# Performance work log

Hardware: AMD Instinct MI355X
Metric: run time of the kernel (lower is better)

## Reference

```python
import jax, jax.numpy as jnp
import numpy as np

K_SIZE = 7   # min_kernel_size (Parameter init value, clamped)
DIL = 2      # min_dilation (Parameter init value, clamped)


def conv2d(x, w, b):
    # x: (B, Cin, H, W), w: (Cout, Cin, kh, kw), stride 1, pad 1
    y = jax.lax.conv_general_dilated(
        x, w, window_strides=(1, 1), padding=((1, 1), (1, 1)),
        dimension_numbers=("NCHW", "OIHW", "NCHW"))
    return y + b[None, :, None, None]


def sincos_1d(length, dim, dtype):
    # standard sinusoidal encoding: (length, dim)
    half = dim // 2
    inv_freq = 1.0 / (10000.0 ** (jnp.arange(half, dtype=dtype) * 2.0 / dim))
    ang = jnp.arange(length, dtype=dtype)[:, None] * inv_freq[None, :]
    return jnp.concatenate([jnp.sin(ang), jnp.cos(ang)], axis=-1)


def positional_encoding_2d(H, W, C, dtype):
    # first C//2 channels encode height, last C//2 encode width -> (H, W, C)
    pe_h = sincos_1d(H, C // 2, dtype)  # (H, C/2)
    pe_w = sincos_1d(W, C // 2, dtype)  # (W, C/2)
    pe = jnp.concatenate([
        jnp.broadcast_to(pe_h[:, None, :], (H, W, C // 2)),
        jnp.broadcast_to(pe_w[None, :, :], (H, W, C // 2)),
    ], axis=-1)
    return pe


def na_indices(L, K, D):
    # NATTEN-style dilated neighborhood indices with border clamping.
    # Each position i attends within its dilation group g = i % D.
    i = jnp.arange(L)
    g = i % D
    r = i // D                       # rank within group
    Lg = (L - g + D - 1) // D        # group length
    start = jnp.clip(r - K // 2, 0, Lg - K)
    return g[:, None] + (start[:, None] + jnp.arange(K)[None, :]) * D  # (L, K)


def neighborhood_attention_2d(q, k, v, K, D):
    # q, k: (B, H, W, Cqk); v: (B, H, W, Cv); single head, scale = Cqk**-0.5
    B, H, W, Cqk = q.shape
    scale = jnp.asarray(Cqk, q.dtype) ** -0.5
    idx_h = na_indices(H, K, D)  # (H, K)
    idx_w = na_indices(W, K, D)  # (W, K)
    # gather neighborhood keys/values: (B, H, K, W, K, C)
    kn = k[:, idx_h][:, :, :, idx_w]
    vn = v[:, idx_h][:, :, :, idx_w]
    logits = jnp.einsum('bhwc,bhiwjc->bhwij', q * scale, kn)  # (B,H,W,K,K)
    p = jax.nn.softmax(logits.reshape(B, H, W, K * K), axis=-1)
    p = p.reshape(B, H, W, K, K)
    return jnp.einsum('bhwij,bhiwjc->bhwc', p, vn)


def setup_inputs() -> dict:
    key = jax.random.key(0)
    ks = jax.random.split(key, 4)
    B, Cin, H, W = 2, 64, 96, 96
    Ci, Co = 64, 128
    fan = Cin * 9
    s = (1.0 / fan) ** 0.5
    return {
        "x": jax.random.normal(ks[0], (B, Cin, H, W), dtype=jnp.float32),
        "wq": jax.random.normal(ks[1], (Ci, Cin, 3, 3), dtype=jnp.float32) * s,
        "bq": jnp.zeros((Ci,), dtype=jnp.float32),
        "wk": jax.random.normal(ks[2], (Ci, Cin, 3, 3), dtype=jnp.float32) * s,
        "bk": jnp.zeros((Ci,), dtype=jnp.float32),
        "wv": jax.random.normal(ks[3], (Co, Cin, 3, 3), dtype=jnp.float32) * s,
        "bv": jnp.zeros((Co,), dtype=jnp.float32),
    }


def reference(x, wq, bq, wk, bk, wv, bv):
    # Conv QKV (NCHW), then move to channels-last for attention
    q = jnp.transpose(conv2d(x, wq, bq), (0, 2, 3, 1))  # (B,H,W,Ci)
    k = jnp.transpose(conv2d(x, wk, bk), (0, 2, 3, 1))
    v = jnp.transpose(conv2d(x, wv, bv), (0, 2, 3, 1))  # (B,H,W,Co)
    B, H, W, Ci = q.shape
    pe = positional_encoding_2d(H, W, Ci, q.dtype)       # (H,W,Ci)
    pe_b = jnp.broadcast_to(pe[None], (B, H, W, Ci))
    q = jnp.concatenate([q, pe_b], axis=-1)              # (B,H,W,2*Ci)
    k = jnp.concatenate([k, pe_b], axis=-1)
    return neighborhood_attention_2d(q, k, v, K_SIZE, DIL)
```

## Files before the change

kernel.cpp:

```cpp
#include <hip/hip_runtime.h>
#include <math.h>

#define HWDIM 96
#define NPIX (HWDIM*HWDIM)
#define BATCH 2
#define CIN 64
#define CCAT 128
#define PADW 98

typedef __attribute__((ext_vector_type(8))) short bf16x8;
typedef __attribute__((ext_vector_type(4))) float f32x4;

__device__ __forceinline__ unsigned short f2bf(float f) {
    unsigned u = __builtin_bit_cast(unsigned, f);
    unsigned r = (u + 0x7FFFu + ((u >> 16) & 1u)) >> 16;
    return (unsigned short)r;
}

__global__ __launch_bounds__(256) void prep_kernel(
        const float* __restrict__ x,
        const float* __restrict__ wq, const float* __restrict__ wk,
        const float* __restrict__ wv,
        unsigned short* __restrict__ xp, unsigned short* __restrict__ wbT) {
    int bid = blockIdx.x;
    int tid = threadIdx.x;
    if (bid < BATCH * PADW) {
        __shared__ float xls[64][97];
        int b  = bid / PADW;
        int hp = bid % PADW;
        bool interior = (hp >= 1 && hp <= HWDIM);
        if (interior) {
            int h = hp - 1;
            for (int idx = tid; idx < 64 * HWDIM; idx += 256) {
                int ci = idx / HWDIM;
                int w  = idx % HWDIM;
                xls[ci][w] = x[((b * CIN + ci) * HWDIM + h) * HWDIM + w];
            }
        }
        __syncthreads();
        for (int idx = tid; idx < PADW * 64; idx += 256) {
            int wp = idx / 64;
            int ci = idx % 64;
            float v = 0.f;
            if (interior && wp >= 1 && wp <= HWDIM) v = xls[ci][wp - 1];
            xp[((b * PADW + hp) * PADW + wp) * 64 + ci] = f2bf(v);
        }
    } else {
        int base = (bid - BATCH * PADW) * 4096;
        #pragma unroll
        for (int e = 0; e < 16; ++e) {
            int idx = base + e * 256 + tid;
            int t   = idx / (256 * 64);
            int rem = idx % (256 * 64);
            int co  = rem / 64;
            int ci  = rem % 64;
            float val;
            if (co < 64)        val = wq[(co * 64 + ci) * 9 + t];
            else if (co < 128)  val = wk[((co - 64) * 64 + ci) * 9 + t];
            else                val = wv[((co - 128) * 64 + ci) * 9 + t];
            wbT[(t * 256 + co) * 64 + ci] = f2bf(val);
        }
    }
}

__global__ __launch_bounds__(256, 2) void conv_mfma(
        const unsigned short* __restrict__ xp,
        const unsigned short* __restrict__ wbT,
        const float* __restrict__ bq, const float* __restrict__ bk,
        const float* __restrict__ bv,
        unsigned short* __restrict__ Qb, unsigned short* __restrict__ Kb,
        unsigned short* __restrict__ Vb) {
    __shared__ unsigned short xs[3 * 50 * 72];
    int bx      = blockIdx.x;
    int spatial = (bx & 7) * 48 + (bx >> 3);
    int b    = spatial / 192;
    int hh   = spatial % 192;
    int h    = hh >> 1;
    int w0   = (hh & 1) * 48;
    int co0  = blockIdx.y * 128;
    int tid  = threadIdx.x;

    {
        uint4 rv[5];
        int   ldst[5];
        #pragma unroll
        for (int i = 0; i < 5; ++i) {
            int idx = tid + i * 256;
            bool valid = (i < 4) || (tid < 176);
            int r    = idx / 400;
            int rem  = idx % 400;
            int wp50 = rem >> 3;
            int c8   = rem & 7;
            if (valid)
                rv[i] = *(const uint4*)&xp[(((b * PADW) + h + r) * PADW + w0 + wp50) * 64 + c8 * 8];
            ldst[i] = (r * 50 + wp50) * 72 + c8 * 8;
        }
        #pragma unroll
        for (int i = 0; i < 5; ++i) {
            bool valid = (i < 4) || (tid < 176);
            if (valid) *(uint4*)&xs[ldst[i]] = rv[i];
        }
    }
    __syncthreads();

    int lane = tid & 63;
    int wv   = tid >> 6;
    int lw   = lane & 15;
    int ksub = (lane >> 4) * 8;
    int co_t = co0 + wv * 32;

    f32x4 acc[3][2];
    #pragma unroll
    for (int m = 0; m < 3; ++m)
        #pragma unroll
        for (int n = 0; n < 2; ++n) acc[m][n] = (f32x4){0.f, 0.f, 0.f, 0.f};

    #pragma unroll
    for (int half = 0; half < 2; ++half) {
        bf16x8 Bf[9][2];
        #pragma unroll
        for (int t = 0; t < 9; ++t) {
            const unsigned short* bp = wbT + ((t * 256 + co_t + lw) * 64) + half * 32 + ksub;
            Bf[t][0] = *(const bf16x8*)(bp);
            Bf[t][1] = *(const bf16x8*)(bp + 16 * 64);
        }
        #pragma unroll
        for (int t = 0; t < 9; ++t) {
            int kh = t / 3, kw = t % 3;
            const unsigned short* ap = xs + (kh * 50 + lw + kw) * 72 + half * 32 + ksub;
            bf16x8 A0 = *(const bf16x8*)(ap);
            bf16x8 A1 = *(const bf16x8*)(ap + 16 * 72);
            bf16x8 A2 = *(const bf16x8*)(ap + 32 * 72);
            acc[0][0] = __builtin_amdgcn_mfma_f32_16x16x32_bf16(A0, Bf[t][0], acc[0][0], 0, 0, 0);
            acc[0][1] = __builtin_amdgcn_mfma_f32_16x16x32_bf16(A0, Bf[t][1], acc[0][1], 0, 0, 0);
            acc[1][0] = __builtin_amdgcn_mfma_f32_16x16x32_bf16(A1, Bf[t][0], acc[1][0], 0, 0, 0);
            acc[1][1] = __builtin_amdgcn_mfma_f32_16x16x32_bf16(A1, Bf[t][1], acc[1][1], 0, 0, 0);
            acc[2][0] = __builtin_amdgcn_mfma_f32_16x16x32_bf16(A2, Bf[t][0], acc[2][0], 0, 0, 0);
            acc[2][1] = __builtin_amdgcn_mfma_f32_16x16x32_bf16(A2, Bf[t][1], acc[2][1], 0, 0, 0);
        }
    }

    __syncthreads();
    unsigned short* xs2 = xs;
    #pragma unroll
    for (int n = 0; n < 2; ++n) {
        int co_f = co_t + n * 16 + lw;
        float bval;
        if (co_f < 64)       bval = bq[co_f];
        else if (co_f < 128) bval = bk[co_f - 64];
        else                 bval = bv[co_f - 128];
        int chl = wv * 32 + n * 16 + lw;
        #pragma unroll
        for (int m = 0; m < 3; ++m) {
            int px = m * 16 + ((lane >> 4) << 2);
            #pragma unroll
            for (int r = 0; r < 4; ++r)
                xs2[(px + r) * 136 + chl] = f2bf(acc[m][n][r] + bval);
        }
    }
    __syncthreads();

    for (int i = tid; i < 768; i += 256) {
        int px  = i >> 4;
        int seg = i & 15;
        uint4 v = *(uint4*)&xs2[px * 136 + seg * 8];
        int pix = b * NPIX + h * HWDIM + w0 + px;
        int chl = seg * 8;
        if (co0 == 0) {
            if (chl < 64) *(uint4*)&Qb[pix * CCAT + chl]        = v;
            else          *(uint4*)&Kb[pix * CCAT + (chl - 64)] = v;
        } else {
            *(uint4*)&Vb[pix * CCAT + chl] = v;
        }
    }

    if (blockIdx.y == 0) {
        for (int i = tid; i < 48 * 64; i += 256) {
            int c  = i & 63;
            int pl = i >> 6;
            int w  = w0 + pl;
            int pos = (c < 32) ? h : w;
            int j   = c & 15;
            float f   = exp2f(-(float)j * 0.83048202372184059f);
            float ang = (float)pos * f;
            float val = ((c & 16) == 0) ? __sinf(ang) : __cosf(ang);
            unsigned short bvv = f2bf(val);
            int pix = b * NPIX + h * HWDIM + w;
            Qb[pix * CCAT + 64 + c] = bvv;
            Kb[pix * CCAT + 64 + c] = bvv;
        }
    }
}

#define KPAD 136
#define LGP  114

__global__ __launch_bounds__(256, 3) void natt_mfma(
        const unsigned short* __restrict__ Qb,
        const unsigned short* __restrict__ Kb,
        const unsigned short* __restrict__ Vb,
        float* __restrict__ out) {
    __shared__ unsigned short Vt[128 * KPAD];
    __shared__ unsigned short Pb[16 * KPAD];
    __shared__ float Lg[16 * LGP];

    int bid  = blockIdx.x;
    int xcd  = bid & 7;
    int slot = bid >> 3;
    int s3   = slot % 3;
    int rest = slot / 3;
    int code = xcd * 3 + s3;
    int b  = code / 12;
    int th = code % 12;
    int tw = rest % 12;
    int gg = rest / 12;
    int gh = gg & 1;
    int gw = gg >> 1;

    int rh0 = th * 4, rw0 = tw * 4;
    int base_h = min(max(rh0 - 3, 0), 41);
    int base_w = min(max(rw0 - 3, 0), 41);
    int tid = threadIdx.x;
    int lane = tid & 63;
    int wv   = tid >> 6;
    int lw   = lane & 15;
    int ks8  = (lane >> 4) * 8;

    uint4 va[4], vb2[4];
    int   vdst[4];
    #pragma unroll
    for (int j = 0; j < 4; ++j) {
        int c = tid + j * 256;
        bool valid = (j < 3) || (tid < 32);
        int pp = c >> 4, c8 = c & 15;
        int px0 = pp * 2, px1 = px0 + 1;
        int ih0 = px0 / 10, iw0 = px0 - ih0 * 10;
        int ih1 = px1 / 10, iw1 = px1 - ih1 * 10;
        int gp0 = b * NPIX + (gh + 2 * min(base_h + ih0, 47)) * HWDIM + (gw + 2 * min(base_w + iw0, 47));
        int gp1 = b * NPIX + (gh + 2 * min(base_h + ih1, 47)) * HWDIM + (gw + 2 * min(base_w + iw1, 47));
        if (valid) {
            va[j]  = *(const uint4*)(Vb + gp0 * CCAT + c8 * 8);
            vb2[j] = *(const uint4*)(Vb + gp1 * CCAT + c8 * 8);
        }
        vdst[j] = (c8 * 8) * KPAD + (px0 ^ ((c8 & 7) << 3));
    }

    for (int i = tid; i < 1024; i += 256) {
        int row = i >> 3, sg = i & 7;
        *(uint4*)(Vt + row * KPAD + 64 + sg * 8) = (uint4){0, 0, 0, 0};
    }

    const float scale = 0.08838834764831845f;
    {
        int qi = lw >> 2, qj = lw & 3;
        const unsigned short* qsrc = Qb +
            ((b * NPIX + (gh + 2 * (rh0 + qi)) * HWDIM + (gw + 2 * (rw0 + qj))) * CCAT) + ks8;
        bf16x8 A0 = *(const bf16x8*)(qsrc);
        bf16x8 A1 = *(const bf16x8*)(qsrc + 32);
        bf16x8 A2 = *(const bf16x8*)(qsrc + 64);
        bf16x8 A3 = *(const bf16x8*)(qsrc + 96);

        #pragma unroll
        for (int tt = 0; tt < 2; ++tt) {
            int tile = wv + tt * 4;
            if (tile < 7) {
                int px = min(tile * 16 + lw, 99);
                int ih = px / 10, iw = px - ih * 10;
                const unsigned short* ksrc = Kb +
                    ((b * NPIX + (gh + 2 * min(base_h + ih, 47)) * HWDIM
                               + (gw + 2 * min(base_w + iw, 47))) * CCAT) + ks8;
                bf16x8 B0 = *(const bf16x8*)(ksrc);
                bf16x8 B1 = *(const bf16x8*)(ksrc + 32);
                bf16x8 B2 = *(const bf16x8*)(ksrc + 64);
                bf16x8 B3 = *(const bf16x8*)(ksrc + 96);
                f32x4 acc = (f32x4){0.f, 0.f, 0.f, 0.f};
                __builtin_amdgcn_s_setprio(1);
                acc = __builtin_amdgcn_mfma_f32_16x16x32_bf16(A0, B0, acc, 0, 0, 0);
                acc = __builtin_amdgcn_mfma_f32_16x16x32_bf16(A1, B1, acc, 0, 0, 0);
                acc = __builtin_amdgcn_mfma_f32_16x16x32_bf16(A2, B2, acc, 0, 0, 0);
                acc = __builtin_amdgcn_mfma_f32_16x16x32_bf16(A3, B3, acc, 0, 0, 0);
                __builtin_amdgcn_s_setprio(0);
                #pragma unroll
                for (int r = 0; r < 4; ++r) {
                    int m = (lane >> 4) * 4 + r;
                    Lg[m * LGP + tile * 16 + lw] = acc[r] * scale;
                }
            }
        }
    }
    __syncthreads();

    #pragma unroll
    for (int j = 0; j < 4; ++j) {
        bool valid = (j < 3) || (tid < 32);
        if (valid) {
            unsigned short* vp = Vt + vdst[j];
            uint4 v0 = va[j], v1 = vb2[j];
            *(unsigned*)(vp + 0 * KPAD) = (v0.x & 0xFFFFu) | (v1.x << 16);
            *(unsigned*)(vp + 1 * KPAD) = (v0.x >> 16)     | (v1.x & 0xFFFF0000u);
            *(unsigned*)(vp + 2 * KPAD) = (v0.y & 0xFFFFu) | (v1.y << 16);
            *(unsigned*)(vp + 3 * KPAD) = (v0.y >> 16)     | (v1.y & 0xFFFF0000u);
            *(unsigned*)(vp + 4 * KPAD) = (v0.z & 0xFFFFu) | (v1.z << 16);
            *(unsigned*)(vp + 5 * KPAD) = (v0.z >> 16)     | (v1.z & 0xFFFF0000u);
            *(unsigned*)(vp + 6 * KPAD) = (v0.w & 0xFFFFu) | (v1.w << 16);
            *(unsigned*)(vp + 7 * KPAD) = (v0.w >> 16)     | (v1.w & 0xFFFF0000u);
        }
    }

    int q   = tid >> 4, k16 = tid & 15;
    {
        int qi  = q >> 2, qj = q & 3;
        int rh  = rh0 + qi, rw = rw0 + qj;
        int oh  = min(max(rh - 3, 0), 41) - base_h;
        int ow  = min(max(rw - 3, 0), 41) - base_w;

        float ev[4];
        int   en[4];
        float mx = -1e30f;
        #pragma unroll
        for (int u = 0; u < 4; ++u) {
            int idx = k16 + u * 16;
            if (idx < 49) {
                int i = idx / 7, j = idx - i * 7;
                int n = (oh + i) * 10 + ow + j;
                en[u] = n;
                float l = Lg[q * LGP + n];
                ev[u] = l;
                mx = fmaxf(mx, l);
            } else { en[u] = -1; ev[u] = 0.f; }
        }
        #pragma unroll
        for (int off = 8; off > 0; off >>= 1) mx = fmaxf(mx, __shfl_xor(mx, off));
        float s = 0.f;
        #pragma unroll
        for (int u = 0; u < 4; ++u)
            if (en[u] >= 0) { ev[u] = __expf(ev[u] - mx); s += ev[u]; }
        #pragma unroll
        for (int off = 8; off > 0; off >>= 1) s += __shfl_xor(s, off);
        float rs = 1.0f / s;
        *(uint4*)(Pb + q * KPAD + k16 * 8) = (uint4){0, 0, 0, 0};
        #pragma unroll
        for (int u = 0; u < 4; ++u)
            if (en[u] >= 0) Pb[q * KPAD + en[u]] = f2bf(ev[u] * rs);
    }
    __syncthreads();

    bf16x8 A4[4];
    #pragma unroll
    for (int kk = 0; kk < 4; ++kk)
        A4[kk] = *(const bf16x8*)(Pb + lw * KPAD + kk * 32 + ks8);

    __builtin_amdgcn_s_setprio(1);
    #pragma unroll
    for (int tt = 0; tt < 2; ++tt) {
        int tile = wv * 2 + tt;
        int row  = tile * 16 + lw;
        int sw   = ((row >> 3) & 7) << 3;
        const unsigned short* vrow = Vt + row * KPAD;
        f32x4 acc = (f32x4){0.f, 0.f, 0.f, 0.f};
        #pragma unroll
        for (int kk = 0; kk < 4; ++kk) {
            bf16x8 Bf = *(const bf16x8*)(vrow + ((kk * 32 + ks8) ^ sw));
            acc = __builtin_amdgcn_mfma_f32_16x16x32_bf16(A4[kk], Bf, acc, 0, 0, 0);
        }
        int ch = row;
        #pragma unroll
        for (int r = 0; r < 4; ++r) {
            int qq = (lane >> 4) * 4 + r;
            int qi = qq >> 2, qj = qq & 3;
            int gp = b * NPIX + (gh + 2 * (rh0 + qi)) * HWDIM + (gw + 2 * (rw0 + qj));
            out[gp * CCAT + ch] = acc[r];
        }
    }
    __builtin_amdgcn_s_setprio(0);
}

extern "C" void kernel_launch(void* const* d_in, const int* in_sizes, int n_in,
                              void* d_out, int out_size, void* d_ws, size_t ws_size,
                              hipStream_t stream) {
    const float* x  = (const float*)d_in[0];
    const float* wq = (const float*)d_in[1];
    const float* bq = (const float*)d_in[2];
    const float* wk = (const float*)d_in[3];
    const float* bk = (const float*)d_in[4];
    const float* wv = (const float*)d_in[5];
    const float* bv = (const float*)d_in[6];

    unsigned short* ws = (unsigned short*)d_ws;
    unsigned short* Qb  = ws;
    unsigned short* Kb  = Qb + BATCH * NPIX * CCAT;
    unsigned short* Vb  = Kb + BATCH * NPIX * CCAT;
    unsigned short* xp  = Vb + BATCH * NPIX * CCAT;
    unsigned short* wbT = xp + BATCH * PADW * PADW * 64;

    hipLaunchKernelGGL(prep_kernel, dim3(BATCH * PADW + 36), dim3(256), 0, stream,
                       x, wq, wk, wv, xp, wbT);
    hipLaunchKernelGGL(conv_mfma, dim3(384, 2), dim3(256), 0, stream,
                       xp, wbT, bq, bk, bv, Qb, Kb, Vb);
    hipLaunchKernelGGL(natt_mfma, dim3(1152), dim3(256), 0, stream,
                       Qb, Kb, Vb, (float*)d_out);
}
```

Before: 43.60 us.

## Fuse input padding and bf16 conversion into conv kernel tile load

Removes the padded channels-last bf16 copy of x that the prep kernel produced. The conv kernel now reads fp32 NCHW x directly, handles the zero-padding borders inline, converts to bf16 and scatters into its shared-memory tile. The weight transposition stays in a small separate kernel. This saves an intermediate global write and read of the padded input. In exchange the loads become scalar fp32 with scattered 2-byte LDS stores, and each block re-reads halo rows that neighbouring blocks also load.

Result: slower. 45.26 us (+3.8%).

```diff
diff --git a/kernel.cpp b/kernel.cpp
--- a/kernel.cpp
+++ b/kernel.cpp
@@ -6,7 +6,6 @@
 #define BATCH 2
 #define CIN 64
 #define CCAT 128
-#define PADW 98
 
 typedef __attribute__((ext_vector_type(8))) short bf16x8;
 typedef __attribute__((ext_vector_type(4))) float f32x4;
@@ -17,54 +16,28 @@
     return (unsigned short)r;
 }
 
-__global__ __launch_bounds__(256) void prep_kernel(
+__global__ __launch_bounds__(256) void wb_kernel(
+        const float* __restrict__ wq, const float* __restrict__ wk,
+        const float* __restrict__ wv, unsigned short* __restrict__ wbT) {
+    int base = blockIdx.x * 4096;
+    int tid  = threadIdx.x;
+    #pragma unroll
+    for (int e = 0; e < 16; ++e) {
+        int idx = base + e * 256 + tid;
+        int t   = idx / (256 * 64);
+        int rem = idx % (256 * 64);
+        int co  = rem / 64;
+        int ci  = rem % 64;
+        float val;
+        if (co < 64)        val = wq[(co * 64 + ci) * 9 + t];
+        else if (co < 128)  val = wk[((co - 64) * 64 + ci) * 9 + t];
+        else                val = wv[((co - 128) * 64 + ci) * 9 + t];
+        wbT[(t * 256 + co) * 64 + ci] = f2bf(val);
+    }
+}
+
+__global__ __launch_bounds__(256, 2) void conv_mfma(
         const float* __restrict__ x,
-        const float* __restrict__ wq, const float* __restrict__ wk,
-        const float* __restrict__ wv,
-        unsigned short* __restrict__ xp, unsigned short* __restrict__ wbT) {
-    int bid = blockIdx.x;
-    int tid = threadIdx.x;
-    if (bid < BATCH * PADW) {
-        __shared__ float xls[64][97];
-        int b  = bid / PADW;
-        int hp = bid % PADW;
-        bool interior = (hp >= 1 && hp <= HWDIM);
-        if (interior) {
-            int h = hp - 1;
-            for (int idx = tid; idx < 64 * HWDIM; idx += 256) {
-                int ci = idx / HWDIM;
-                int w  = idx % HWDIM;
-                xls[ci][w] = x[((b * CIN + ci) * HWDIM + h) * HWDIM + w];
-            }
-        }
-        __syncthreads();
-        for (int idx = tid; idx < PADW * 64; idx += 256) {
-            int wp = idx / 64;
-            int ci = idx % 64;
-            float v = 0.f;
-            if (interior && wp >= 1 && wp <= HWDIM) v = xls[ci][wp - 1];
-            xp[((b * PADW + hp) * PADW + wp) * 64 + ci] = f2bf(v);
-        }
-    } else {
-        int base = (bid - BATCH * PADW) * 4096;
-        #pragma unroll
-        for (int e = 0; e < 16; ++e) {
-            int idx = base + e * 256 + tid;
-            int t   = idx / (256 * 64);
-            int rem = idx % (256 * 64);
-            int co  = rem / 64;
-            int ci  = rem % 64;
-            float val;
-            if (co < 64)        val = wq[(co * 64 + ci) * 9 + t];
-            else if (co < 128)  val = wk[((co - 64) * 64 + ci) * 9 + t];
-            else                val = wv[((co - 128) * 64 + ci) * 9 + t];
-            wbT[(t * 256 + co) * 64 + ci] = f2bf(val);
-        }
-    }
-}
-
-__global__ __launch_bounds__(256, 2) void conv_mfma(
-        const unsigned short* __restrict__ xp,
         const unsigned short* __restrict__ wbT,
         const float* __restrict__ bq, const float* __restrict__ bk,
         const float* __restrict__ bv,
@@ -80,26 +53,31 @@
     int co0  = blockIdx.y * 128;
     int tid  = threadIdx.x;
 
-    {
-        uint4 rv[5];
-        int   ldst[5];
-        #pragma unroll
-        for (int i = 0; i < 5; ++i) {
-            int idx = tid + i * 256;
-            bool valid = (i < 4) || (tid < 176);
-            int r    = idx / 400;
-            int rem  = idx % 400;
-            int wp50 = rem >> 3;
-            int c8   = rem & 7;
-            if (valid)
-                rv[i] = *(const uint4*)&xp[(((b * PADW) + h + r) * PADW + w0 + wp50) * 64 + c8 * 8];
-            ldst[i] = (r * 50 + wp50) * 72 + c8 * 8;
-        }
-        #pragma unroll
-        for (int i = 0; i < 5; ++i) {
-            bool valid = (i < 4) || (tid < 176);
-            if (valid) *(uint4*)&xs[ldst[i]] = rv[i];
-        }
+    #pragma unroll
+    for (int g = 0; g < 5; ++g) {
+        float vv[8];
+        int   dst[8];
+        bool  ok[8];
+        #pragma unroll
+        for (int e = 0; e < 8; ++e) {
+            int i  = tid + (g * 8 + e) * 256;
+            ok[e]  = (i < 9600);
+            int ii = ok[e] ? i : 0;
+            int r   = ii / 3200;
+            int rem = ii % 3200;
+            int ci  = rem / 50;
+            int px  = rem % 50;
+            int iy  = h - 1 + r;
+            int ix  = w0 - 1 + px;
+            float v = 0.f;
+            if (ok[e] && iy >= 0 && iy < HWDIM && ix >= 0 && ix < HWDIM)
+                v = x[((b * CIN + ci) * HWDIM + iy) * HWDIM + ix];
+            vv[e]  = v;
+            dst[e] = (r * 50 + px) * 72 + ci;
+        }
+        #pragma unroll
+        for (int e = 0; e < 8; ++e)
+            if (ok[e]) xs[dst[e]] = f2bf(vv[e]);
     }
     __syncthreads();
 
@@ -390,13 +368,12 @@
     unsigned short* Qb  = ws;
     unsigned short* Kb  = Qb + BATCH * NPIX * CCAT;
     unsigned short* Vb  = Kb + BATCH * NPIX * CCAT;
-    unsigned short* xp  = Vb + BATCH * NPIX * CCAT;
-    unsigned short* wbT = xp + BATCH * PADW * PADW * 64;
-
-    hipLaunchKernelGGL(prep_kernel, dim3(BATCH * PADW + 36), dim3(256), 0, stream,
-                       x, wq, wk, wv, xp, wbT);
+    unsigned short* wbT = Vb + BATCH * NPIX * CCAT;
+
+    hipLaunchKernelGGL(wb_kernel, dim3(36), dim3(256), 0, stream,
+                       wq, wk, wv, wbT);
     hipLaunchKernelGGL(conv_mfma, dim3(384, 2), dim3(256), 0, stream,
-                       xp, wbT, bq, bk, bv, Qb, Kb, Vb);
+                       x, wbT, bq, bk, bv, Qb, Kb, Vb);
     hipLaunchKernelGGL(natt_mfma, dim3(1152), dim3(256), 0, stream,
                        Qb, Kb, Vb, (float*)d_out);
 }
```
